# Kernel optimization log

Hardware: AMD Instinct MI355X
Metric: run time of the kernel (lower is better)

Reference implementation:

```python
import jax, jax.numpy as jnp
import numpy as np

TRIANGLE_TABLE = np.array([
    [-1, -1, -1, -1, -1, -1], [1, 0, 2, -1, -1, -1], [4, 0, 3, -1, -1, -1], [1, 4, 2, 1, 3, 4],
    [3, 1, 5, -1, -1, -1], [2, 3, 0, 2, 5, 3], [1, 4, 0, 1, 5, 4], [4, 2, 5, -1, -1, -1],
    [4, 5, 2, -1, -1, -1], [4, 1, 0, 4, 5, 1], [3, 2, 0, 3, 5, 2], [1, 3, 5, -1, -1, -1],
    [4, 1, 2, 4, 3, 1], [3, 0, 4, -1, -1, -1], [2, 0, 1, -1, -1, -1], [-1, -1, -1, -1, -1, -1]], np.int32)
NUM_TRIANGLES_TABLE = np.array([0, 1, 1, 2, 1, 2, 2, 1, 1, 2, 2, 1, 2, 1, 1, 0], np.int32)
BASE_TET_EDGES = np.array([0, 1, 0, 2, 0, 3, 1, 2, 1, 3, 2, 3], np.int32)


def _make_tet_grid(R):
    # Regular grid in [0,1]^3, each cube split into 6 tets along the 0-7 diagonal.
    r1 = R + 1
    gi, gj, gk = np.meshgrid(np.arange(r1), np.arange(r1), np.arange(r1), indexing='ij')
    verts = (np.stack([gi, gj, gk], -1).reshape(-1, 3) / R).astype(np.float32)  # (Nv,3)
    ci, cj, ck = np.meshgrid(np.arange(R), np.arange(R), np.arange(R), indexing='ij')
    ci, cj, ck = ci.ravel(), cj.ravel(), ck.ravel()
    def vid(dx, dy, dz):
        return ((ci + dx) * r1 + (cj + dy)) * r1 + (ck + dz)
    corners = [vid((c >> 2) & 1, (c >> 1) & 1, c & 1) for c in range(8)]
    tet_corners = [(0, 1, 3, 7), (0, 3, 2, 7), (0, 2, 6, 7), (0, 6, 4, 7), (0, 4, 5, 7), (0, 5, 1, 7)]
    tets = np.stack([np.stack([corners[a] for a in t], -1) for t in tet_corners], 1).reshape(-1, 4)
    return verts, tets.astype(np.int32)


def setup_inputs() -> dict:
    R = 64
    verts, tets = _make_tet_grid(R)
    key = jax.random.key(0)
    k1, k2 = jax.random.split(key)
    level = jax.random.normal(k1, (verts.shape[0],), dtype=jnp.float32)
    deformation = jax.random.normal(k2, (verts.shape[0], 3), dtype=jnp.float32)
    return {
        'level': level,
        'deformation': deformation,
        'grid_vertices': jnp.asarray(verts),
        'tet_indices': jnp.asarray(tets),
        'resolution': R,
    }


def reference(level, deformation, grid_vertices, tet_indices, resolution):
    # normalize_grid_deformation: (range_hi - range_lo)/res * tanh(offsets), range = (0,1)
    pos = grid_vertices + jnp.tanh(deformation) / resolution  # (Nv,3)
    occ = level > 0                                           # (Nv,)
    occ_f = occ[tet_indices]                                  # (F,4)
    occ_sum = occ_f.sum(-1)
    valid = (occ_sum > 0) & (occ_sum < 4)
    vt = tet_indices[valid]                                   # (Fv,4)
    occ_valid = occ_f[valid]                                  # (Fv,4)
    # per-tet edges, each sorted (min,max) -> dedup
    edges = vt[:, jnp.asarray(BASE_TET_EDGES)].reshape(-1, 2)  # (6*Fv,2)
    edges = jnp.sort(edges, axis=1)
    unique_edges, idx_map = jnp.unique(edges, axis=0, return_inverse=True)
    idx_map = idx_map.reshape(-1)
    # edges that actually cross the isosurface (exactly one endpoint inside)
    mask_edges = occ[unique_edges].sum(-1) == 1               # (U,)
    mapping = jnp.where(mask_edges, jnp.cumsum(mask_edges.astype(jnp.int32)) - 1, -1)
    idx_map = mapping[idx_map].reshape(-1, 6)                 # (Fv,6)
    interp_v = unique_edges[mask_edges]                       # (M,2)
    # linear interpolation of crossing point along each edge
    ep = pos[interp_v]                                        # (M,2,3)
    es = level[interp_v] * jnp.array([1.0, -1.0], dtype=level.dtype)  # (M,2) = [sdf0, -sdf1]
    w = es[:, ::-1] / es.sum(1, keepdims=True)                # (M,2) = [-sdf1, sdf0]/(sdf0-sdf1)
    verts_out = (ep * w[:, :, None]).sum(1)                   # (M,3)
    # triangle table lookup
    v_id = jnp.array([1, 2, 4, 8], dtype=jnp.int32)
    tetindex = (occ_valid.astype(jnp.int32) * v_id).sum(-1)   # (Fv,)
    tri_tab = jnp.asarray(TRIANGLE_TABLE)
    num_tri = jnp.asarray(NUM_TRIANGLES_TABLE)[tetindex]
    m1 = num_tri == 1
    m2 = num_tri == 2
    f1 = jnp.take_along_axis(idx_map[m1], tri_tab[tetindex[m1]][:, :3], axis=1).reshape(-1, 3)
    f2 = jnp.take_along_axis(idx_map[m2], tri_tab[tetindex[m2]][:, :6], axis=1).reshape(-1, 3)
    faces = jnp.concatenate([f1, f2], axis=0)                 # (Nf,3)
    return verts_out, faces
```

## Files before the change

kernel.cpp:

```cpp
#include <hip/hip_runtime.h>
#include <math.h>


typedef unsigned long long ull;

#define ST_LD(p)    __hip_atomic_load((p), __ATOMIC_RELAXED, __HIP_MEMORY_SCOPE_AGENT)
#define ST_ST(p,v)  __hip_atomic_store((p), (v), __ATOMIC_RELAXED, __HIP_MEMORY_SCOPE_AGENT)

__device__ __forceinline__ float fast_tanh(float x) {
    float e = __expf(2.0f * x);
    return __fdividef(e - 1.0f, e + 1.0f);
}

__device__ __forceinline__ int divq(unsigned v, ull M) {
    return (int)(((ull)v * M) >> 46);
}

constexpr int TT[16][6] = {
    {-1,-1,-1,-1,-1,-1},{1,0,2,-1,-1,-1},{4,0,3,-1,-1,-1},{1,4,2,1,3,4},
    {3,1,5,-1,-1,-1},{2,3,0,2,5,3},{1,4,0,1,5,4},{4,2,5,-1,-1,-1},
    {4,5,2,-1,-1,-1},{4,1,0,4,5,1},{3,2,0,3,5,2},{1,3,5,-1,-1,-1},
    {4,1,2,4,3,1},{3,0,4,-1,-1,-1},{2,0,1,-1,-1,-1},{-1,-1,-1,-1,-1,-1}};
constexpr int NTRI[16] = {0,1,1,2,1,2,2,1,1,2,2,1,2,1,1,0};
constexpr int TC[6][4] = {{0,1,3,7},{0,3,2,7},{0,2,6,7},{0,6,4,7},{0,4,5,7},{0,5,1,7}};
constexpr int TE[6][6] = {
    {(0<<3)|0,(0<<3)|2,(0<<3)|6,(1<<3)|1,(1<<3)|5,(3<<3)|3},
    {(0<<3)|2,(0<<3)|1,(0<<3)|6,(2<<3)|0,(3<<3)|3,(2<<3)|4},
    {(0<<3)|1,(0<<3)|5,(0<<3)|6,(2<<3)|3,(2<<3)|4,(6<<3)|0},
    {(0<<3)|5,(0<<3)|3,(0<<3)|6,(4<<3)|1,(6<<3)|0,(4<<3)|2},
    {(0<<3)|3,(0<<3)|4,(0<<3)|6,(4<<3)|0,(4<<3)|2,(5<<3)|1},
    {(0<<3)|4,(0<<3)|0,(0<<3)|6,(1<<3)|3,(5<<3)|1,(1<<3)|5}};

struct DTabT { ull w[2048]; };
constexpr DTabT make_dtab() {
    DTabT t{};
    for (int ob = 0; ob < 256; ob++) {
        for (int k = 0; k < 8; k++) {
            ull w = 0;
            if (k < 6) {
                int ti = ((ob >> TC[k][0]) & 1) | (((ob >> TC[k][1]) & 1) << 1)
                       | (((ob >> TC[k][2]) & 1) << 2) | (((ob >> TC[k][3]) & 1) << 3);
                int nt = NTRI[ti];
                int pre1 = 0, pre2 = 0;
                for (int kk = 0; kk < k; kk++) {
                    int tik = ((ob >> TC[kk][0]) & 1) | (((ob >> TC[kk][1]) & 1) << 1)
                            | (((ob >> TC[kk][2]) & 1) << 2) | (((ob >> TC[kk][3]) & 1) << 3);
                    pre1 += (NTRI[tik] == 1); pre2 += (NTRI[tik] == 2);
                }
                w = (ull)nt | ((ull)pre1 << 2) | ((ull)pre2 << 5);
                for (int e = 0; e < 6; e++) {
                    int le = TT[ti][e];
                    int ce = (le >= 0) ? TE[k][le] : 0;
                    w |= (ull)ce << (8 + 6 * e);
                }
            }
            t.w[ob * 8 + k] = w;
        }
    }
    return t;
}
__device__ __constant__ DTabT c_dtab = make_dtab();

#define TAG      (1ull << 62)
#define PMASK    ((1ull << 60) - 1ull)
#define READY(s) (((s) >> 62) == 1ull)

__device__ __forceinline__ unsigned sel8(int c, unsigned r0, unsigned r1_, unsigned r2,
                                         unsigned r3, unsigned r4, unsigned r5,
                                         unsigned r6, unsigned r7) {
    unsigned a01 = (c & 1) ? r1_ : r0;
    unsigned a23 = (c & 1) ? r3 : r2;
    unsigned a45 = (c & 1) ? r5 : r4;
    unsigned a67 = (c & 1) ? r7 : r6;
    unsigned lo = (c & 2) ? a23 : a01;
    unsigned hi = (c & 2) ? a67 : a45;
    return (c & 4) ? hi : lo;
}

__global__ __launch_bounds__(256, 4) void k_all(
        const float* __restrict__ level, const float* __restrict__ deform,
        int NV, int NC, int r1, float invR,
        ull Mrsq, ull Mr1, ull Mrr, ull MR, int FOFF,
        ull* __restrict__ stateA, ull* __restrict__ flagF, ull* __restrict__ totalsF,
        unsigned* __restrict__ rankWord, ull* __restrict__ cubeInfo,
        float* __restrict__ out) {
    __shared__ float ldsB[9216];
    __shared__ int wE[4], wT[4];
    __shared__ ull sPart[4];
    __shared__ unsigned sB1, sB2, sE1, sE2;
    __shared__ ull sTot;

    int b = blockIdx.x, tid = threadIdx.x;
    int v = b * 256 + tid;
    int R = r1 - 1, rsq = r1 * r1, rr = R * R;

    bool valid = v < NV;
    float la = valid ? level[v] : 0.f;
    bool occv = valid && (la > 0.f);

    int x = 0, y = 0, z = 0, flags = 0, n1 = 0, n2 = 0, cidx = 0, ob = 0;
    bool interior = false;
    float lb[7];
    if (valid) {
        x = divq((unsigned)v, Mrsq); int rem = v - x * rsq;
        y = divq((unsigned)rem, Mr1); z = rem - y * r1;
        bool bx = x < R, by = y < R, bz = z < R;
        interior = bx && by && bz;
        bool inb[7] = {bz, by, by && bz, bx, bx && bz, bx && by, interior};
        int deltas[7] = {1, r1, r1 + 1, rsq, rsq + 1, rsq + r1, rsq + r1 + 1};
        ob = occv ? 1 : 0;
        #pragma unroll
        for (int j = 0; j < 7; j++) {
            float l = inb[j] ? level[v + deltas[j]] : 0.f;
            lb[j] = l;
            bool o = inb[j] && (l > 0.f);
            ob |= (o ? 1 : 0) << (j + 1);
            if (inb[j] && (o != occv)) flags |= 1 << j;
        }
        if (interior) {
            cidx = ((x * R) + y) * R + z;
            #pragma unroll
            for (int k = 0; k < 6; k++) {
                int ti = ((ob >> TC[k][0]) & 1) | (((ob >> TC[k][1]) & 1) << 1)
                       | (((ob >> TC[k][2]) & 1) << 2) | (((ob >> TC[k][3]) & 1) << 3);
                int p = __popc(ti);
                n1 += (p == 1) || (p == 3);
                n2 += (p == 2);
            }
        }
    }
    int cnt = __popc(flags);
    int pk = n1 | (n2 << 16);
    int lane = tid & 63, wv = tid >> 6;
    int inclE = cnt, inclT = pk;
    #pragma unroll
    for (int o = 1; o < 64; o <<= 1) {
        int tE = __shfl_up(inclE, o);
        int tT = __shfl_up(inclT, o);
        if (lane >= o) { inclE += tE; inclT += tT; }
    }
    if (lane == 63) { wE[wv] = inclE; wT[wv] = inclT; }
    __syncthreads();

    if (tid == 0) {
        int eb = wE[0] + wE[1] + wE[2] + wE[3];
        int tb = wT[0] + wT[1] + wT[2] + wT[3];
        ST_ST(&stateA[b], TAG | ((ull)eb << 40) | ((ull)(tb & 0xffff) << 20) | (ull)(tb >> 16));
    }
    int woffE = 0, woffT = 0;
    for (int w2 = 0; w2 < wv; w2++) { woffE += wE[w2]; woffT += wT[w2]; }
    int localRank = woffE + inclE - cnt;
    int tExcl = woffT + inclT - pk;

    if (flags) {
        int deltas[7] = {1, r1, r1 + 1, rsq, rsq + 1, rsq + r1, rsq + r1 + 1};
        const int dxs[7] = {0, 0, 0, 1, 1, 1, 1};
        const int dys[7] = {0, 1, 1, 0, 0, 1, 1};
        const int dzs[7] = {1, 0, 1, 0, 1, 0, 1};
        float pax = x * invR + fast_tanh(deform[3 * v])     * invR;
        float pay = y * invR + fast_tanh(deform[3 * v + 1]) * invR;
        float paz = z * invR + fast_tanh(deform[3 * v + 2]) * invR;
        int r = localRank;
        #pragma unroll
        for (int j = 0; j < 7; j++) {
            if ((flags >> j) & 1) {
                int bb = v + deltas[j];
                float lbv = lb[j];
                float inv = __fdividef(1.0f, la - lbv);
                float w0 = -lbv * inv;
                float w1f = la * inv;
                float pbx = (x + dxs[j]) * invR + fast_tanh(deform[3 * bb])     * invR;
                float pby = (y + dys[j]) * invR + fast_tanh(deform[3 * bb + 1]) * invR;
                float pbz = (z + dzs[j]) * invR + fast_tanh(deform[3 * bb + 2]) * invR;
                ldsB[3 * r]     = pax * w0 + pbx * w1f;
                ldsB[3 * r + 1] = pay * w0 + pby * w1f;
                ldsB[3 * r + 2] = paz * w0 + pbz * w1f;
                r++;
            }
        }
    }

    ull psum = 0;
    for (int t = 0;; t++) {
        int base = 64 * (4 * t + wv);
        if (base >= b) break;
        int i = b - 1 - (base + lane);
        ull s = 0;
        if (i >= 0) {
            for (;;) {
                s = ST_LD(&stateA[i]);
                if (READY(s)) break;
                __builtin_amdgcn_s_sleep(1);
            }
            s &= PMASK;
        }
        psum += s;
    }
    #pragma unroll
    for (int o = 1; o < 64; o <<= 1) psum += __shfl_xor(psum, o);
    if (lane == 0) sPart[wv] = psum;
    __syncthreads();

    ull ex = sPart[0] + sPart[1] + sPart[2] + sPart[3];
    int exclE = (int)((ex >> 40) & 0xFFFFF);
    int excl1 = (int)((ex >> 20) & 0xFFFFF);
    int excl2 = (int)(ex & 0xFFFFF);
    int eb2 = wE[0] + wE[1] + wE[2] + wE[3];
    if (tid == 0 && b == (int)gridDim.x - 1) {
        int tb = wT[0] + wT[1] + wT[2] + wT[3];
        ull inc = ex + (((ull)eb2 << 40) | ((ull)(tb & 0xffff) << 20) | (ull)(tb >> 16));
        ST_ST(totalsF, TAG | inc);
    }
    if (interior)
        ST_ST(&cubeInfo[cidx],
              (ull)(unsigned)ob
            | ((ull)(unsigned)(excl1 + (tExcl & 0xffff)) << 8)
            | ((ull)(unsigned)(excl2 + (tExcl >> 16)) << 28));
    if (valid)
        ST_ST(&rankWord[v], (unsigned)(exclE + localRank) | ((unsigned)flags << 21));

    __syncthreads();
    if (tid == 0)
        ST_ST(&flagF[b], TAG | 1ull);

    {
        int tot = 3 * eb2;
        float* dstV = out + 3 * (size_t)exclE;
        for (int i = tid; i < tot; i += 256) dstV[i] = ldsB[i];
    }
    __syncthreads();

    int fb = b - FOFF;
    if (fb >= 0) {
        int c = fb * 256 + tid;
        bool act = c < NC;

        int c0 = fb * 256;
        int c1e = c0 + 255; if (c1e > NC - 1) c1e = NC - 1;
        int cx0 = divq((unsigned)c0, Mrr); int rem0 = c0 - cx0 * rr;
        int cy0 = divq((unsigned)rem0, MR);
        int vlo = (cx0 * r1 + cy0) * r1 + (rem0 - cy0 * R);
        int cx1 = divq((unsigned)c1e, Mrr); int rem1 = c1e - cx1 * rr;
        int cy1 = divq((unsigned)rem1, MR);
        int vhi = (cx1 * r1 + cy1) * r1 + (rem1 - cy1 * R) + rsq + r1 + 1;
        int vbLo = vlo >> 8, vbHi = vhi >> 8;
        if (tid <= vbHi - vbLo) {
            for (;;) {
                ull f = ST_LD(&flagF[vbLo + tid]);
                if (READY(f)) break;
                __builtin_amdgcn_s_sleep(1);
            }
        }
        __syncthreads();

        ull info = 0;
        ull w0 = 0, w1 = 0, w2 = 0, w3 = 0, w4 = 0, w5 = 0;
        unsigned rw0=0,rw1=0,rw2=0,rw3=0,rw4=0,rw5=0,rw6=0,rw7=0;
        if (act) {
            info = ST_LD(&cubeInfo[c]);
            int obf = (int)info & 255;
            const ull* dp = &c_dtab.w[obf << 3];
            ulonglong2 p0 = *reinterpret_cast<const ulonglong2*>(dp);
            ulonglong2 p1 = *reinterpret_cast<const ulonglong2*>(dp + 2);
            ulonglong2 p2 = *reinterpret_cast<const ulonglong2*>(dp + 4);
            w0 = p0.x; w1 = p0.y; w2 = p1.x; w3 = p1.y; w4 = p2.x; w5 = p2.y;
            int cx = divq((unsigned)c, Mrr); int rem = c - cx * rr;
            int cy = divq((unsigned)rem, MR); int cz = rem - cy * R;
            int vc = (cx * r1 + cy) * r1 + cz;
            rw0 = ST_LD(&rankWord[vc]);             rw1 = ST_LD(&rankWord[vc + 1]);
            rw2 = ST_LD(&rankWord[vc + r1]);        rw3 = ST_LD(&rankWord[vc + r1 + 1]);
            rw4 = ST_LD(&rankWord[vc + rsq]);       rw5 = ST_LD(&rankWord[vc + rsq + 1]);
            rw6 = ST_LD(&rankWord[vc + rsq + r1]);  rw7 = ST_LD(&rankWord[vc + rsq + r1 + 1]);
        }
        unsigned r1c = (unsigned)((info >> 8) & 0xFFFFF);
        unsigned r2c = (unsigned)((info >> 28) & 0xFFFFF);
        int nt5 = (int)w5 & 3;
        int n1c = (((int)w5 >> 2) & 7) + (nt5 == 1);
        int n2c = (((int)w5 >> 5) & 7) + (nt5 == 2);

        int lastT = NC - 1 - fb * 256; if (lastT > 255) lastT = 255;
        if (tid == 0)     { sB1 = r1c; sB2 = r2c; }
        if (tid == lastT) { sE1 = r1c + (unsigned)n1c; sE2 = r2c + (unsigned)n2c; }
        __syncthreads();

        int n1b = (int)(sE1 - sB1), n2b = (int)(sE2 - sB2);
        float* Lr1 = ldsB;
        float* Lr2 = ldsB + 3 * n1b;

        #define ERANK(ce_)                                                      \
            ({ int ce = (ce_);                                                  \
               unsigned rw = sel8(ce >> 3, rw0,rw1,rw2,rw3,rw4,rw5,rw6,rw7);    \
               (float)((int)(rw & 0x1FFFFF) + __popc((rw >> 21) & ((1u << (ce & 7)) - 1u))); })

        if (act) {
            int local1 = (int)(r1c - sB1);
            int local2 = (int)(r2c - sB2);
            #define DO_TET(wk) do {                                             \
                int nt = (int)(wk) & 3;                                         \
                if (nt) {                                                       \
                    ull we = (wk) >> 8;                                         \
                    if (nt == 1) {                                              \
                        int s = local1 + (((int)(wk) >> 2) & 7);                \
                        float* d = &Lr1[3 * s];                                 \
                        d[0] = ERANK((int)(we) & 63);                           \
                        d[1] = ERANK((int)(we >> 6) & 63);                      \
                        d[2] = ERANK((int)(we >> 12) & 63);                     \
                    } else {                                                    \
                        int s = local2 + (((int)(wk) >> 5) & 7);                \
                        float* d = &Lr2[6 * s];                                 \
                        d[0] = ERANK((int)(we) & 63);                           \
                        d[1] = ERANK((int)(we >> 6) & 63);                      \
                        d[2] = ERANK((int)(we >> 12) & 63);                     \
                        d[3] = ERANK((int)(we >> 18) & 63);                     \
                        d[4] = ERANK((int)(we >> 24) & 63);                     \
                        d[5] = ERANK((int)(we >> 30) & 63);                     \
                    }                                                           \
                }                                                               \
            } while (0)
            DO_TET(w0); DO_TET(w1); DO_TET(w2); DO_TET(w3); DO_TET(w4); DO_TET(w5);
            #undef DO_TET
        }
        #undef ERANK

        if (tid == 0) {
            ull t;
            for (;;) {
                t = ST_LD(totalsF);
                if (READY(t)) break;
                __builtin_amdgcn_s_sleep(8);
            }
            sTot = t;
        }
        __syncthreads();

        ull tot = sTot;
        int M  = (int)((tot >> 40) & 0xFFFFF);
        int N1 = (int)((tot >> 20) & 0xFFFFF);
        float* faces = out + 3 * (size_t)M;
        float* d1 = faces + 3 * (size_t)sB1;
        for (int i = tid; i < 3 * n1b; i += 256) d1[i] = ldsB[i];
        float* d2 = faces + 3 * (size_t)N1 + 6 * (size_t)sB2;
        const float* s2 = ldsB + 3 * n1b;
        for (int i = tid; i < 6 * n2b; i += 256) d2[i] = s2[i];
    }
}

extern "C" void kernel_launch(void* const* d_in, const int* in_sizes, int n_in,
                              void* d_out, int out_size, void* d_ws, size_t ws_size,
                              hipStream_t stream) {
    const float* level  = (const float*)d_in[0];
    const float* deform = (const float*)d_in[1];
    int NV = in_sizes[0];
    int r1 = 1;
    while ((long long)r1 * r1 * r1 < (long long)NV) r1++;
    int R = r1 - 1;
    float invR = 1.0f / (float)R;
    int rsq = r1 * r1, rr = R * R;

    ull Mrsq = ((1ull << 46) + (ull)rsq - 1) / (ull)rsq;
    ull Mr1  = ((1ull << 46) + (ull)r1  - 1) / (ull)r1;
    ull Mrr  = ((1ull << 46) + (ull)rr  - 1) / (ull)rr;
    ull MR   = ((1ull << 46) + (ull)R   - 1) / (ull)R;

    int nb = (NV + 255) / 256;
    int NC = R * R * R;
    int nbC = (NC + 255) / 256;
    int FOFF = nb - nbC;

    char* w = (char*)d_ws;
    unsigned* rankWord = (unsigned*)w;
    w += (((size_t)NV * sizeof(unsigned)) + 255) & ~(size_t)255;
    ull* cubeInfo = (ull*)w;
    w += (((size_t)NC * 8) + 255) & ~(size_t)255;
    ull* stateA = (ull*)w;
    w += (((size_t)nb * 8) + 255) & ~(size_t)255;
    ull* flagF = (ull*)w;
    w += (((size_t)nb * 8) + 255) & ~(size_t)255;
    ull* totalsF = (ull*)w;

    float* out = (float*)d_out;

    k_all<<<nb, 256, 0, stream>>>(level, deform, NV, NC, r1, invR,
                                  Mrsq, Mr1, Mrr, MR, FOFF,
                                  stateA, flagF, totalsF, rankWord, cubeInfo, out);
}
```

Baseline: 110.8 us.

## Stage face output in workspace and copy via second kernel instead of spin-waiting

Face-producing blocks no longer spin-wait for the last block to publish global totals. They write their triangles to workspace buffers for one-triangle and two-triangle faces, and a second kernel reads the totals and copies both buffers into their final offsets in the output. This removes a grid-wide dependency on the last block, but adds an extra kernel launch and a second pass that reads and writes the face data through global memory.

New measurement: 120.6 us. +8.8%, slower.

```diff
diff --git a/kernel.cpp b/kernel.cpp
--- a/kernel.cpp
+++ b/kernel.cpp
@@ -80,15 +80,15 @@
 __global__ __launch_bounds__(256, 4) void k_all(
         const float* __restrict__ level, const float* __restrict__ deform,
         int NV, int NC, int r1, float invR,
-        ull Mrsq, ull Mr1, ull Mrr, ull MR, int FOFF,
-        ull* __restrict__ stateA, ull* __restrict__ flagF, ull* __restrict__ totalsF,
+        ull Mrsq, ull Mr1, ull Mrr, ull MR, int XB,
+        ull* __restrict__ stateA, ull* __restrict__ flagF, int* __restrict__ totals,
         unsigned* __restrict__ rankWord, ull* __restrict__ cubeInfo,
+        float* __restrict__ wsF1, float* __restrict__ wsF2,
         float* __restrict__ out) {
     __shared__ float ldsB[9216];
     __shared__ int wE[4], wT[4];
     __shared__ ull sPart[4];
     __shared__ unsigned sB1, sB2, sE1, sE2;
-    __shared__ ull sTot;
 
     int b = blockIdx.x, tid = threadIdx.x;
     int v = b * 256 + tid;
@@ -209,7 +209,9 @@
     if (tid == 0 && b == (int)gridDim.x - 1) {
         int tb = wT[0] + wT[1] + wT[2] + wT[3];
         ull inc = ex + (((ull)eb2 << 40) | ((ull)(tb & 0xffff) << 20) | (ull)(tb >> 16));
-        ST_ST(totalsF, TAG | inc);
+        totals[0] = (int)((inc >> 40) & 0xFFFFF);
+        totals[1] = (int)((inc >> 20) & 0xFFFFF);
+        totals[2] = (int)(inc & 0xFFFFF);
     }
     if (interior)
         ST_ST(&cubeInfo[cidx],
@@ -230,7 +232,7 @@
     }
     __syncthreads();
 
-    int fb = b - FOFF;
+    int fb = b - XB;
     if (fb >= 0) {
         int c = fb * 256 + tid;
         bool act = c < NC;
@@ -321,28 +323,28 @@
             #undef DO_TET
         }
         #undef ERANK
-
-        if (tid == 0) {
-            ull t;
-            for (;;) {
-                t = ST_LD(totalsF);
-                if (READY(t)) break;
-                __builtin_amdgcn_s_sleep(8);
-            }
-            sTot = t;
-        }
         __syncthreads();
 
-        ull tot = sTot;
-        int M  = (int)((tot >> 40) & 0xFFFFF);
-        int N1 = (int)((tot >> 20) & 0xFFFFF);
-        float* faces = out + 3 * (size_t)M;
-        float* d1 = faces + 3 * (size_t)sB1;
+        float* d1 = wsF1 + 3 * (size_t)sB1;
         for (int i = tid; i < 3 * n1b; i += 256) d1[i] = ldsB[i];
-        float* d2 = faces + 3 * (size_t)N1 + 6 * (size_t)sB2;
+        float* d2 = wsF2 + 6 * (size_t)sB2;
         const float* s2 = ldsB + 3 * n1b;
         for (int i = tid; i < 6 * n2b; i += 256) d2[i] = s2[i];
     }
+}
+
+__global__ __launch_bounds__(256) void k_copy(
+        const int* __restrict__ totals,
+        const float* __restrict__ wsF1, const float* __restrict__ wsF2,
+        float* __restrict__ out) {
+    int M = totals[0], N1 = totals[1], N2 = totals[2];
+    size_t n1f = 3 * (size_t)N1;
+    size_t n2f = 6 * (size_t)N2;
+    size_t total = n1f + n2f;
+    float* faces = out + 3 * (size_t)M;
+    size_t stride = (size_t)gridDim.x * 256;
+    for (size_t i = (size_t)blockIdx.x * 256 + threadIdx.x; i < total; i += stride)
+        faces[i] = (i < n1f) ? wsF1[i] : wsF2[i - n1f];
 }
 
 extern "C" void kernel_launch(void* const* d_in, const int* in_sizes, int n_in,
@@ -365,7 +367,7 @@
     int nb = (NV + 255) / 256;
     int NC = R * R * R;
     int nbC = (NC + 255) / 256;
-    int FOFF = nb - nbC;
+    int XB = nb - nbC;
 
     char* w = (char*)d_ws;
     unsigned* rankWord = (unsigned*)w;
@@ -376,11 +378,17 @@
     w += (((size_t)nb * 8) + 255) & ~(size_t)255;
     ull* flagF = (ull*)w;
     w += (((size_t)nb * 8) + 255) & ~(size_t)255;
-    ull* totalsF = (ull*)w;
+    int* totals = (int*)w;
+    w += 256;
+    float* wsF1 = (float*)w;
+    w += (((size_t)NC * 6 * 3 * 4) + 255) & ~(size_t)255;
+    float* wsF2 = (float*)w;
 
     float* out = (float*)d_out;
 
     k_all<<<nb, 256, 0, stream>>>(level, deform, NV, NC, r1, invR,
-                                  Mrsq, Mr1, Mrr, MR, FOFF,
-                                  stateA, flagF, totalsF, rankWord, cubeInfo, out);
-}
+                                  Mrsq, Mr1, Mrr, MR, XB,
+                                  stateA, flagF, totals, rankWord, cubeInfo,
+                                  wsF1, wsF2, out);
+    k_copy<<<2048, 256, 0, stream>>>(totals, wsF1, wsF2, out);
+}
```
